# Kernel tuning notes

Measured on AMD Instinct MI355X. Metric: run time of the kernel, lower is better.

## Reference

```python
import jax, jax.numpy as jnp
import numpy as np

B, S, I, H = 32, 1024, 512, 512


def setup_inputs() -> dict:
    key = jax.random.key(0)
    ks = jax.random.split(key, 4)
    stdv = 1.0 / np.sqrt(H)
    return {
        "inputs": jax.random.normal(ks[0], (B, S, I), dtype=jnp.float32),
        "h0": jnp.zeros((1, B, H), dtype=jnp.float32),
        "c0": jnp.zeros((1, B, H), dtype=jnp.float32),
        "weight_ih": jax.random.uniform(ks[1], (4 * H, I), jnp.float32, -stdv, stdv),
        "weight_hh": jax.random.uniform(ks[2], (4 * H, H), jnp.float32, -stdv, stdv),
        "bias_ih": jax.random.uniform(ks[3], (4 * H,), jnp.float32, -stdv, stdv),
        "bias_hh": jax.random.uniform(jax.random.fold_in(key, 7), (4 * H,), jnp.float32, -stdv, stdv),
    }


def _lstm(inputs, h0, c0, weight_ih, weight_hh, bias_ih, bias_hh):
    # Precompute input projections for all timesteps: [B,S,4H]
    x_proj = jnp.einsum('bsi,gi->bsg', inputs, weight_ih) + bias_ih + bias_hh
    h_init = h0[0]  # [B,H]
    c_init = c0[0]  # [B,H]
    hidden = h_init.shape[-1]

    def step(carry, xg):
        h, c = carry
        gates = xg + h @ weight_hh.T  # [B,4H]
        i_t = jax.nn.sigmoid(gates[:, 0 * hidden:1 * hidden])
        f_t = jax.nn.sigmoid(gates[:, 1 * hidden:2 * hidden])
        g_t = jnp.tanh(gates[:, 2 * hidden:3 * hidden])
        o_t = jax.nn.sigmoid(gates[:, 3 * hidden:4 * hidden])
        c_new = f_t * c + i_t * g_t
        h_new = o_t * jnp.tanh(c_new)
        return (h_new, c_new), h_new

    (hn, cn), outs = jax.lax.scan(step, (h_init, c_init), jnp.swapaxes(x_proj, 0, 1))
    outputs = jnp.swapaxes(outs, 0, 1)  # [B,S,H]
    return outputs, hn[None], cn[None]


def reference(inputs, h0, c0, weight_ih, weight_hh, bias_ih, bias_hh):
    return _lstm(inputs, h0, c0, weight_ih, weight_hh, bias_ih, bias_hh)
```

## Files before the change

kernel.cpp:

```cpp
#include <hip/hip_runtime.h>
#include <cstddef>
#include <cstdint>

#define HID   512
#define G4    2048
#define NB    32
#define SEQL  1024
#define INPD  512
#define NBLK  128
#define TPB   512

typedef _Float16 half8 __attribute__((ext_vector_type(8)));
typedef float    f32x4 __attribute__((ext_vector_type(4)));

__device__ __forceinline__ float sigm(float x) {
    return 1.0f / (1.0f + __expf(-x));
}
__device__ __forceinline__ float tanh_fast(float x) {
    float e = __expf(-2.0f * fabsf(x));
    float t = (1.0f - e) / (1.0f + e);
    return copysignf(t, x);
}

__device__ __forceinline__ int orig_gate(int gp) {
    int r = gp & 15;
    return (r >> 2) * HID + (gp >> 4) * 4 + (r & 3);
}

__global__ __launch_bounds__(256) void conv_whh(const float* __restrict__ whh,
                                                _Float16* __restrict__ wh) {
    int e = blockIdx.x * 256 + threadIdx.x;
    int R = e >> 9, k = e & 511;
    int ty = R >> 9, rem = R & 511;
    int j = rem >> 2, uu = rem & 3;
    int p = uu * 4 + ty;
    wh[((size_t)j * 16 + p) * 512 + k] = (_Float16)whh[e];
}

__global__ __launch_bounds__(256) void conv_wih(const float* __restrict__ wih,
                                                _Float16* __restrict__ wi) {
    int e = blockIdx.x * 256 + threadIdx.x;
    int R = e >> 9, k = e & 511;
    int ty = R >> 9, u = R & 511;
    int j = u >> 2, uu = u & 3;
    int gp = j * 16 + ty * 4 + uu;
    wi[(size_t)gp * 512 + k] = (_Float16)wih[e];
}

__global__ __launch_bounds__(256) void conv_bias(const float* __restrict__ bih,
                                                 const float* __restrict__ bhh,
                                                 float* __restrict__ bp) {
    int gp = blockIdx.x * 256 + threadIdx.x;
    int og = orig_gate(gp);
    bp[gp] = bih[og] + bhh[og];
}

__global__ __launch_bounds__(256) void conv_xh(const float* __restrict__ x,
                                               _Float16* __restrict__ xh) {
    int i = blockIdx.x * 256 + threadIdx.x;
    const float4* s = (const float4*)(x + (size_t)i * 8);
    float4 a = s[0], b = s[1];
    half8 v = {(_Float16)a.x, (_Float16)a.y, (_Float16)a.z, (_Float16)a.w,
               (_Float16)b.x, (_Float16)b.y, (_Float16)b.z, (_Float16)b.w};
    *(half8*)(xh + (size_t)i * 8) = v;
}

__global__ __launch_bounds__(256) void xproj_mfma(const _Float16* __restrict__ xh,
                                                  const _Float16* __restrict__ wi,
                                                  const float* __restrict__ bp,
                                                  float* __restrict__ xbuf,
                                                  int chunk, int SC) {
    __shared__ __align__(16) _Float16 As[64 * 36];
    __shared__ __align__(16) _Float16 Bs[64 * 36];

    const int m0 = blockIdx.x * 64;
    const int n0 = blockIdx.y * 64;
    const int t  = threadIdx.x;
    const int w  = t >> 6, lane = t & 63;

    const int sr = t >> 2, sq = (t & 3) * 8;
    const int m  = m0 + sr;
    const int b  = m / SC, tl = m % SC;
    const _Float16* arow = xh + ((size_t)b * SEQL + (size_t)chunk * SC + tl) * INPD + sq;
    const _Float16* brow = wi + (size_t)(n0 + sr) * 512 + sq;

    const int arow_l = 16 * w + (lane & 15);
    const int kl     = (lane >> 4) * 8;

    float bias[4];
    #pragma unroll
    for (int nt = 0; nt < 4; ++nt)
        bias[nt] = bp[n0 + nt * 16 + (lane & 15)];

    f32x4 acc[4] = {};
    for (int kk = 0; kk < 16; ++kk) {
        *(half8*)&As[sr * 36 + sq] = *(const half8*)(arow + kk * 32);
        *(half8*)&Bs[sr * 36 + sq] = *(const half8*)(brow + kk * 32);
        __syncthreads();
        half8 av = *(const half8*)&As[arow_l * 36 + kl];
        #pragma unroll
        for (int nt = 0; nt < 4; ++nt) {
            half8 bv = *(const half8*)&Bs[(nt * 16 + (lane & 15)) * 36 + kl];
            acc[nt] = __builtin_amdgcn_mfma_f32_16x16x32_f16(av, bv, acc[nt], 0, 0, 0);
        }
        __syncthreads();
    }

    #pragma unroll
    for (int nt = 0; nt < 4; ++nt) {
        int n = n0 + nt * 16 + (lane & 15);
        #pragma unroll
        for (int reg = 0; reg < 4; ++reg) {
            int mg = m0 + 16 * w + (lane >> 4) * 4 + reg;
            xbuf[(size_t)mg * G4 + n] = acc[nt][reg] + bias[nt];
        }
    }
}

__global__ __launch_bounds__(512, 1)
void lstm_persist(const _Float16* __restrict__ wh,
                  const float* __restrict__ xbuf,
                  const float* __restrict__ c0,
                  unsigned long long* __restrict__ hbuf,
                  float* __restrict__ cstate,
                  float* __restrict__ out,
                  int* __restrict__ flags,
                  int step_base, int SC) {
    __shared__ __align__(16) _Float16 h_lds[32 * 520];
    __shared__ __align__(16) float    part[32 * 67];
    __shared__ __align__(16) float    gl[32 * 20];

    const int j  = blockIdx.x;
    const int t  = threadIdx.x;
    const int u0 = 4 * j;

    const int w    = t >> 6, lane = t & 63;
    const int mt   = w & 1, kg = w >> 1;
    const int arow = 16 * mt + (lane & 15);
    const int p_b  = lane & 15;
    const int kl   = (lane >> 4) * 8;

    const int mt_r = t & 1;
    const int idx  = t >> 1;
    const int n_r  = idx & 15;
    const int m_r  = idx >> 4;
    const int b_t  = 16 * mt_r + m_r;
    const int lsrc = (m_r >> 2) * 16 + n_r;
    const int regr = m_r & 3;
    const int xcol = 16 * j + (n_r & 3) * 4 + (n_r >> 2);

    half8 wf[4];
    {
        const _Float16* wrow = wh + ((size_t)j * 16 + p_b) * 512 + kg * 128 + kl;
        #pragma unroll
        for (int q = 0; q < 4; ++q)
            wf[q] = *(const half8*)(wrow + q * 32);
    }

    float cA = 0.0f, cB = 0.0f;
    const int b_c = t & 31, pp = t >> 5;
    if (t < 64) {
        const float* cs = (step_base == 0 ? c0 : cstate) + b_c * HID + u0 + 2 * pp;
        float2 cv = *(const float2*)cs;
        cA = cv.x; cB = cv.y;
    }

    for (int s = 0; s < SC; ++s) {
        const int g = step_base + s;

        float xg = xbuf[((size_t)b_t * SC + s) * G4 + xcol];

        const unsigned long long* hs8 = hbuf + (size_t)(g & 1) * 4096;
        #pragma unroll
        for (int i = 0; i < 4; ++i) {
            unsigned long long va = __hip_atomic_load(hs8 + i * 1024 + 2 * t,
                                                      __ATOMIC_RELAXED,
                                                      __HIP_MEMORY_SCOPE_AGENT);
            unsigned long long vb = __hip_atomic_load(hs8 + i * 1024 + 2 * t + 1,
                                                      __ATOMIC_RELAXED,
                                                      __HIP_MEMORY_SCOPE_AGENT);
            int j16 = i * 512 + t;
            int br = j16 >> 6, k16 = j16 & 63;
            uint4 v;
            __builtin_memcpy(&v.x, &va, 8);
            __builtin_memcpy(&v.z, &vb, 8);
            *(uint4*)&h_lds[br * 520 + k16 * 8] = v;
        }
        __syncthreads();

        f32x4 acc = {0.f, 0.f, 0.f, 0.f};
        #pragma unroll
        for (int q = 0; q < 4; ++q) {
            const int k = (kg * 4 + q) * 32 + kl;
            half8 av = *(const half8*)&h_lds[arow * 520 + k];
            acc = __builtin_amdgcn_mfma_f32_16x16x32_f16(av, wf[q], acc, 0, 0, 0);
        }
        #pragma unroll
        for (int r = 0; r < 4; ++r)
            part[(r * 8 + w) * 67 + lane] = acc[r];
        __syncthreads();

        float sum = xg;
        #pragma unroll
        for (int kgg = 0; kgg < 4; ++kgg)
            sum += part[(regr * 8 + kgg * 2 + mt_r) * 67 + lsrc];
        gl[b_t * 20 + n_r] = sum;
        __syncthreads();

        float hA = 0.0f, hB = 0.0f;
        if (t < 64) {
            float4 gA = *(const float4*)&gl[b_c * 20 + 8 * pp];
            float4 gB = *(const float4*)&gl[b_c * 20 + 8 * pp + 4];
            cA = fmaf(sigm(gA.y), cA, sigm(gA.x) * tanh_fast(gA.z));
            hA = sigm(gA.w) * tanh_fast(cA);
            cB = fmaf(sigm(gB.y), cB, sigm(gB.x) * tanh_fast(gB.z));
            hB = sigm(gB.w) * tanh_fast(cB);

            _Float16 hv2[2] = {(_Float16)hA, (_Float16)hB};
            unsigned hu;
            __builtin_memcpy(&hu, hv2, 4);
            unsigned* hb32 = (unsigned*)hbuf;
            __hip_atomic_store(hb32 + (size_t)((g + 1) & 1) * 8192
                                    + b_c * 256 + (u0 >> 1) + pp,
                               hu, __ATOMIC_RELAXED, __HIP_MEMORY_SCOPE_AGENT);
        }
        __syncthreads();

        if (t == 0)
            __hip_atomic_store(&flags[j * 32], g + 1,
                               __ATOMIC_RELAXED, __HIP_MEMORY_SCOPE_AGENT);

        if (t < 64) {
            float2 ov; ov.x = hA; ov.y = hB;
            *(float2*)&out[((size_t)b_c * SEQL + g) * HID + u0 + 2 * pp] = ov;
        }

        if (t < NBLK) {
            while (__hip_atomic_load(&flags[t * 32], __ATOMIC_RELAXED,
                                     __HIP_MEMORY_SCOPE_AGENT) < g + 1)
                __builtin_amdgcn_s_sleep(1);
        }
        __syncthreads();
    }

    if (t < 64) {
        float2 cv; cv.x = cA; cv.y = cB;
        *(float2*)&cstate[b_c * HID + u0 + 2 * pp] = cv;
    }
}

__global__ __launch_bounds__(256) void finalize(const _Float16* __restrict__ hfin,
                                                const float* __restrict__ cs,
                                                float* __restrict__ out) {
    int i = blockIdx.x * blockDim.x + threadIdx.x;
    size_t base = (size_t)NB * SEQL * HID;
    if (i < NB * HID) {
        out[base + i] = (float)hfin[i];
        out[base + NB * HID + i] = cs[i];
    }
}

extern "C" void kernel_launch(void* const* d_in, const int* in_sizes, int n_in,
                              void* d_out, int out_size, void* d_ws, size_t ws_size,
                              hipStream_t stream) {
    const float* x   = (const float*)d_in[0];
    const float* h0  = (const float*)d_in[1];
    const float* c0  = (const float*)d_in[2];
    const float* wih = (const float*)d_in[3];
    const float* whh = (const float*)d_in[4];
    const float* bih = (const float*)d_in[5];
    const float* bhh = (const float*)d_in[6];
    float* out = (float*)d_out;

    char* ws = (char*)d_ws;
    size_t off = 0;
    int*       flags  = (int*)(ws + off);        off += 16384;
    _Float16*  hbuf_h = (_Float16*)(ws + off);   off += 65536;
    float*     cstate = (float*)(ws + off);      off += 65536;
    _Float16*  wh_h   = (_Float16*)(ws + off);   off += 2097152;
    _Float16*  wi_h   = (_Float16*)(ws + off);   off += 2097152;
    float*     biasp  = (float*)(ws + off);      off += 8192;
    _Float16*  xh     = (_Float16*)(ws + off);   off += (size_t)NB * SEQL * INPD * 2;
    float*     xbuf   = (float*)(ws + off);

    size_t fixed = off;
    int SC = SEQL;
    while (SC > 64 && fixed + (size_t)NB * SC * G4 * sizeof(float) > ws_size) SC >>= 1;

    hipMemsetAsync(flags, 0, 16384, stream);
    conv_whh<<<(2048 * 512) / 256, 256, 0, stream>>>(whh, wh_h);
    conv_wih<<<(2048 * 512) / 256, 256, 0, stream>>>(wih, wi_h);
    conv_bias<<<2048 / 256, 256, 0, stream>>>(bih, bhh, biasp);
    conv_xh<<<(NB * SEQL * INPD / 8) / 256, 256, 0, stream>>>(x, xh);
    {
    }
    conv_bias<<<1, 1, 0, stream>>>(bih, bhh, biasp);
    {
        static_assert(NB * HID % 256 == 0, "");
    }
    extern __global__ void conv_h0_k(const float*, _Float16*);
    conv_h0_k<<<(NB * HID) / 256, 256, 0, stream>>>(h0, hbuf_h);

    int nchunks = SEQL / SC;
    for (int ch = 0; ch < nchunks; ++ch) {
        dim3 grd(NB * SC / 64, G4 / 64);
        xproj_mfma<<<grd, 256, 0, stream>>>(xh, wi_h, biasp, xbuf, ch, SC);
        lstm_persist<<<NBLK, TPB, 0, stream>>>(wh_h, xbuf, c0,
                                               (unsigned long long*)hbuf_h,
                                               cstate, out, flags, ch * SC, SC);
    }

    finalize<<<(NB * HID + 255) / 256, 256, 0, stream>>>(hbuf_h, cstate, out);
}

__global__ __launch_bounds__(256) void conv_h0_k(const float* __restrict__ h0,
                                                 _Float16* __restrict__ hb) {
    int e = blockIdx.x * 256 + threadIdx.x;
    hb[e] = (_Float16)h0[e];
}
```

Measured before the change: 3.224 ms.

## Replace flag barrier with step-tagged hidden-state words polled directly

Each fp16 hidden value is now stored in a 32-bit word with the step number in the upper 16 bits. Consumers spin on the hidden-state buffer itself until every word carries the expected tag, which removes the separate per-block flag stores, the flag polling loop and two block-wide barriers per timestep. The cost is a doubled hidden buffer, twice the bytes per h load, and per-word tag checks and retries. It also relies on 16-bit step tags and relaxed atomics being enough for correct ordering.

```diff
diff --git a/kernel.cpp b/kernel.cpp
--- a/kernel.cpp
+++ b/kernel.cpp
@@ -65,6 +65,15 @@
     *(half8*)(xh + (size_t)i * 8) = v;
 }
 
+__global__ __launch_bounds__(256) void conv_h0(const float* __restrict__ h0,
+                                               unsigned* __restrict__ hb) {
+    int e = blockIdx.x * 256 + threadIdx.x;
+    _Float16 hh = (_Float16)h0[e];
+    unsigned short u;
+    __builtin_memcpy(&u, &hh, 2);
+    hb[e] = (unsigned)u;
+}
+
 __global__ __launch_bounds__(256) void xproj_mfma(const _Float16* __restrict__ xh,
                                                   const _Float16* __restrict__ wi,
                                                   const float* __restrict__ bp,
@@ -124,7 +133,6 @@
                   unsigned long long* __restrict__ hbuf,
                   float* __restrict__ cstate,
                   float* __restrict__ out,
-                  int* __restrict__ flags,
                   int step_base, int SC) {
     __shared__ __align__(16) _Float16 h_lds[32 * 520];
     __shared__ __align__(16) float    part[32 * 67];
@@ -170,22 +178,43 @@
 
         float xg = xbuf[((size_t)b_t * SC + s) * G4 + xcol];
 
-        const unsigned long long* hs8 = hbuf + (size_t)(g & 1) * 4096;
-        #pragma unroll
-        for (int i = 0; i < 4; ++i) {
-            unsigned long long va = __hip_atomic_load(hs8 + i * 1024 + 2 * t,
-                                                      __ATOMIC_RELAXED,
-                                                      __HIP_MEMORY_SCOPE_AGENT);
-            unsigned long long vb = __hip_atomic_load(hs8 + i * 1024 + 2 * t + 1,
-                                                      __ATOMIC_RELAXED,
-                                                      __HIP_MEMORY_SCOPE_AGENT);
-            int j16 = i * 512 + t;
-            int br = j16 >> 6, k16 = j16 & 63;
-            uint4 v;
-            __builtin_memcpy(&v.x, &va, 8);
-            __builtin_memcpy(&v.z, &vb, 8);
-            *(uint4*)&h_lds[br * 520 + k16 * 8] = v;
-        }
+        const unsigned long long* hs8 = hbuf + (size_t)(g & 1) * 8192;
+        const unsigned long long pat = ((unsigned long long)(unsigned short)g << 48)
+                                     | ((unsigned long long)(unsigned short)g << 16);
+        unsigned long long v0,v1,v2,v3,v4,v5,v6,v7,v8,v9,v10,v11,v12,v13,v14,v15;
+        bool k0,k1,k2,k3,k4,k5,k6,k7,k8,k9,k10,k11,k12,k13,k14,k15;
+        #define LOADQ(i) \
+            v##i = __hip_atomic_load(hs8 + i * 512 + t, __ATOMIC_RELAXED, \
+                                     __HIP_MEMORY_SCOPE_AGENT); \
+            k##i = ((v##i & 0xFFFF0000FFFF0000ull) == pat)
+        LOADQ(0); LOADQ(1); LOADQ(2); LOADQ(3);
+        LOADQ(4); LOADQ(5); LOADQ(6); LOADQ(7);
+        LOADQ(8); LOADQ(9); LOADQ(10); LOADQ(11);
+        LOADQ(12); LOADQ(13); LOADQ(14); LOADQ(15);
+        for (;;) {
+            bool all = k0 & k1 & k2 & k3 & k4 & k5 & k6 & k7
+                     & k8 & k9 & k10 & k11 & k12 & k13 & k14 & k15;
+            if (all) break;
+            __builtin_amdgcn_s_sleep(1);
+            #define RETRYQ(i) if (!k##i) { LOADQ(i); }
+            RETRYQ(0); RETRYQ(1); RETRYQ(2); RETRYQ(3);
+            RETRYQ(4); RETRYQ(5); RETRYQ(6); RETRYQ(7);
+            RETRYQ(8); RETRYQ(9); RETRYQ(10); RETRYQ(11);
+            RETRYQ(12); RETRYQ(13); RETRYQ(14); RETRYQ(15);
+            #undef RETRYQ
+        }
+        #undef LOADQ
+        #define STOREQ(i) { \
+            int j8 = i * 512 + t; \
+            int bq = j8 >> 8, r8 = j8 & 255; \
+            unsigned payload = (unsigned)(v##i & 0xFFFF) \
+                             | (((unsigned)(v##i >> 32) & 0xFFFFu) << 16); \
+            ((unsigned*)h_lds)[bq * 260 + r8] = payload; }
+        STOREQ(0); STOREQ(1); STOREQ(2); STOREQ(3);
+        STOREQ(4); STOREQ(5); STOREQ(6); STOREQ(7);
+        STOREQ(8); STOREQ(9); STOREQ(10); STOREQ(11);
+        STOREQ(12); STOREQ(13); STOREQ(14); STOREQ(15);
+        #undef STOREQ
         __syncthreads();
 
         f32x4 acc = {0.f, 0.f, 0.f, 0.f};
@@ -207,40 +236,28 @@
         gl[b_t * 20 + n_r] = sum;
         __syncthreads();
 
-        float hA = 0.0f, hB = 0.0f;
         if (t < 64) {
             float4 gA = *(const float4*)&gl[b_c * 20 + 8 * pp];
             float4 gB = *(const float4*)&gl[b_c * 20 + 8 * pp + 4];
             cA = fmaf(sigm(gA.y), cA, sigm(gA.x) * tanh_fast(gA.z));
-            hA = sigm(gA.w) * tanh_fast(cA);
+            float hA = sigm(gA.w) * tanh_fast(cA);
             cB = fmaf(sigm(gB.y), cB, sigm(gB.x) * tanh_fast(gB.z));
-            hB = sigm(gB.w) * tanh_fast(cB);
-
-            _Float16 hv2[2] = {(_Float16)hA, (_Float16)hB};
-            unsigned hu;
-            __builtin_memcpy(&hu, hv2, 4);
-            unsigned* hb32 = (unsigned*)hbuf;
-            __hip_atomic_store(hb32 + (size_t)((g + 1) & 1) * 8192
-                                    + b_c * 256 + (u0 >> 1) + pp,
-                               hu, __ATOMIC_RELAXED, __HIP_MEMORY_SCOPE_AGENT);
-        }
-        __syncthreads();
-
-        if (t == 0)
-            __hip_atomic_store(&flags[j * 32], g + 1,
-                               __ATOMIC_RELAXED, __HIP_MEMORY_SCOPE_AGENT);
-
-        if (t < 64) {
+            float hB = sigm(gB.w) * tanh_fast(cB);
+
+            _Float16 ha16 = (_Float16)hA, hb16 = (_Float16)hB;
+            unsigned short hau, hbu;
+            __builtin_memcpy(&hau, &ha16, 2);
+            __builtin_memcpy(&hbu, &hb16, 2);
+            const unsigned tg1 = (unsigned)(unsigned short)(g + 1);
+            unsigned long long pv = ((unsigned long long)((tg1 << 16) | hau))
+                                  | ((unsigned long long)((tg1 << 16) | hbu) << 32);
+            __hip_atomic_store(hbuf + (size_t)((g + 1) & 1) * 8192
+                                    + b_c * 256 + 2 * j + pp,
+                               pv, __ATOMIC_RELAXED, __HIP_MEMORY_SCOPE_AGENT);
+
             float2 ov; ov.x = hA; ov.y = hB;
             *(float2*)&out[((size_t)b_c * SEQL + g) * HID + u0 + 2 * pp] = ov;
         }
-
-        if (t < NBLK) {
-            while (__hip_atomic_load(&flags[t * 32], __ATOMIC_RELAXED,
-                                     __HIP_MEMORY_SCOPE_AGENT) < g + 1)
-                __builtin_amdgcn_s_sleep(1);
-        }
-        __syncthreads();
     }
 
     if (t < 64) {
@@ -249,13 +266,16 @@
     }
 }
 
-__global__ __launch_bounds__(256) void finalize(const _Float16* __restrict__ hfin,
+__global__ __launch_bounds__(256) void finalize(const unsigned* __restrict__ hfin,
                                                 const float* __restrict__ cs,
                                                 float* __restrict__ out) {
     int i = blockIdx.x * blockDim.x + threadIdx.x;
     size_t base = (size_t)NB * SEQL * HID;
     if (i < NB * HID) {
-        out[base + i] = (float)hfin[i];
+        unsigned short u = (unsigned short)(hfin[i] & 0xFFFF);
+        _Float16 hh;
+        __builtin_memcpy(&hh, &u, 2);
+        out[base + i] = (float)hh;
         out[base + NB * HID + i] = cs[i];
     }
 }
@@ -274,8 +294,7 @@
 
     char* ws = (char*)d_ws;
     size_t off = 0;
-    int*       flags  = (int*)(ws + off);        off += 16384;
-    _Float16*  hbuf_h = (_Float16*)(ws + off);   off += 65536;
+    unsigned long long* hbuf = (unsigned long long*)(ws + off); off += 131072;
     float*     cstate = (float*)(ws + off);      off += 65536;
     _Float16*  wh_h   = (_Float16*)(ws + off);   off += 2097152;
     _Float16*  wi_h   = (_Float16*)(ws + off);   off += 2097152;
@@ -287,34 +306,20 @@
     int SC = SEQL;
     while (SC > 64 && fixed + (size_t)NB * SC * G4 * sizeof(float) > ws_size) SC >>= 1;
 
-    hipMemsetAsync(flags, 0, 16384, stream);
     conv_whh<<<(2048 * 512) / 256, 256, 0, stream>>>(whh, wh_h);
     conv_wih<<<(2048 * 512) / 256, 256, 0, stream>>>(wih, wi_h);
     conv_bias<<<2048 / 256, 256, 0, stream>>>(bih, bhh, biasp);
     conv_xh<<<(NB * SEQL * INPD / 8) / 256, 256, 0, stream>>>(x, xh);
-    {
-    }
-    conv_bias<<<1, 1, 0, stream>>>(bih, bhh, biasp);
-    {
-        static_assert(NB * HID % 256 == 0, "");
-    }
-    extern __global__ void conv_h0_k(const float*, _Float16*);
-    conv_h0_k<<<(NB * HID) / 256, 256, 0, stream>>>(h0, hbuf_h);
+    conv_h0<<<(NB * HID) / 256, 256, 0, stream>>>(h0, (unsigned*)hbuf);
 
     int nchunks = SEQL / SC;
     for (int ch = 0; ch < nchunks; ++ch) {
         dim3 grd(NB * SC / 64, G4 / 64);
         xproj_mfma<<<grd, 256, 0, stream>>>(xh, wi_h, biasp, xbuf, ch, SC);
-        lstm_persist<<<NBLK, TPB, 0, stream>>>(wh_h, xbuf, c0,
-                                               (unsigned long long*)hbuf_h,
-                                               cstate, out, flags, ch * SC, SC);
-    }
-
-    finalize<<<(NB * HID + 255) / 256, 256, 0, stream>>>(hbuf_h, cstate, out);
-}
-
-__global__ __launch_bounds__(256) void conv_h0_k(const float* __restrict__ h0,
-                                                 _Float16* __restrict__ hb) {
-    int e = blockIdx.x * 256 + threadIdx.x;
-    hb[e] = (_Float16)h0[e];
-}
+        lstm_persist<<<NBLK, TPB, 0, stream>>>(wh_h, xbuf, c0, hbuf,
+                                               cstate, out, ch * SC, SC);
+    }
+
+    finalize<<<(NB * HID + 255) / 256, 256, 0, stream>>>((const unsigned*)hbuf,
+                                                         cstate, out);
+}
```

Result: slower. 8.244 ms (+155.7%).
